# Optimization experiments

Measured on AMD Instinct MI355X. Metric: run time of the kernel, lower is better.

The kernel has to match this reference:

```python
import jax, jax.numpy as jnp
import numpy as np

D_K = 64

def setup_inputs() -> dict:
    key = jax.random.key(0)
    k1, k2, k3 = jax.random.split(key, 3)
    shape = (4, 16, 2048, D_K)  # [batch, heads, seq, d_k]
    return {
        "q": jax.random.normal(k1, shape, dtype=jnp.float32),
        "k": jax.random.normal(k2, shape, dtype=jnp.float32),
        "v": jax.random.normal(k3, shape, dtype=jnp.float32),
    }

def reference(q, k, v):
    # scores: [B, H, S, S] = Q K^T / sqrt(d_k)
    scale = 1.0 / jnp.sqrt(jnp.asarray(D_K, dtype=q.dtype))
    scores = jnp.einsum("bhqd,bhkd->bhqk", q, k) * scale
    attn = jax.nn.softmax(scores, axis=-1)
    out = jnp.einsum("bhqk,bhkd->bhqd", attn, v)
    return out
```

## Files before the change

### kernel.cpp

```cpp
#include <hip/hip_runtime.h>


#define S_LEN 2048
#define D_K 64
#define BQ 128
#define BK 64
#define NT (S_LEN / BK)
#define LST 72

typedef __attribute__((ext_vector_type(8))) _Float16 fragh;
typedef __attribute__((ext_vector_type(4))) _Float16 half4v;
typedef __attribute__((ext_vector_type(2))) _Float16 half2v;
typedef __attribute__((ext_vector_type(4))) float facc;

__device__ __forceinline__ half2v pkrtz(float a, float b) {
  return __builtin_bit_cast(half2v, __builtin_amdgcn_cvt_pkrtz(a, b));
}

__global__ __launch_bounds__(256, 4) void sdpa_kernel(
    const float* __restrict__ q, const float* __restrict__ k,
    const float* __restrict__ v, float* __restrict__ out) {
  __shared__ _Float16 QP[BQ][LST];
  __shared__ _Float16 Ks[BK][LST];
  __shared__ _Float16 Vs[D_K][LST];

  const int t = threadIdx.x;
  const int wave = t >> 6;
  const int lane = t & 63;
  const int ln15 = lane & 15;
  const int quad = lane >> 4;

  const int bh = blockIdx.y;
  const int q0 = blockIdx.x * BQ;

  const float* qp = q + ((size_t)bh * S_LEN + q0) * D_K;
  const float* kp = k + (size_t)bh * S_LEN * D_K;
  const float* vp = v + (size_t)bh * S_LEN * D_K;

  const float qs = 0.125f * 1.44269504088896340736f;

  #pragma unroll
  for (int i = 0; i < 8; ++i) {
    int e = i * 1024 + t * 4;
    float4 f = *(const float4*)(qp + e);
    int r = e >> 6, c = e & 63;
    half2v a = pkrtz(f.x * qs, f.y * qs);
    half2v b = pkrtz(f.z * qs, f.w * qs);
    *(half4v*)&QP[r][c] = __builtin_shufflevector(a, b, 0, 1, 2, 3);
  }
  __syncthreads();

  fragh qf[2][2];
  #pragma unroll
  for (int mi = 0; mi < 2; ++mi) {
    int row = wave * 32 + mi * 16 + ln15;
    qf[mi][0] = *(const fragh*)&QP[row][quad * 8];
    qf[mi][1] = *(const fragh*)&QP[row][32 + quad * 8];
  }

  fragh ones;
  #pragma unroll
  for (int j = 0; j < 8; ++j) ones[j] = (_Float16)1.0f;

  facc O[2][4];
  facc Ol[2];
  #pragma unroll
  for (int mi = 0; mi < 2; ++mi) {
    Ol[mi] = (facc){0.f, 0.f, 0.f, 0.f};
    #pragma unroll
    for (int r = 0; r < 4; ++r) O[mi][r] = (facc){0.f, 0.f, 0.f, 0.f};
  }

  const int vp0 = ln15 + 16 * (wave & 1);
  const int vg0 = quad + 4 * (wave >> 1);

  float4 kpre[4], vpre[4];
  {
    const float* kb = kp;
    const float* vb = vp;
    #pragma unroll
    for (int i = 0; i < 4; ++i) kpre[i] = *(const float4*)(kb + i * 1024 + t * 4);
    #pragma unroll
    for (int i = 0; i < 2; ++i) {
      const float* vsrc = vb + 2 * vp0 * D_K + 4 * (vg0 + 8 * i);
      vpre[2 * i + 0] = *(const float4*)(vsrc);
      vpre[2 * i + 1] = *(const float4*)(vsrc + D_K);
    }
  }

  for (int kt = 0; kt < NT; ++kt) {
    __syncthreads();

    #pragma unroll
    for (int i = 0; i < 4; ++i) {
      int e = i * 1024 + t * 4;
      int r = e >> 6, c = e & 63;
      half2v a = pkrtz(kpre[i].x, kpre[i].y);
      half2v b = pkrtz(kpre[i].z, kpre[i].w);
      *(half4v*)&Ks[r][c] = __builtin_shufflevector(a, b, 0, 1, 2, 3);
    }
    #pragma unroll
    for (int i = 0; i < 2; ++i) {
      int g = vg0 + 8 * i;
      float4 f0 = vpre[2 * i + 0];
      float4 f1 = vpre[2 * i + 1];
      *(half2v*)&Vs[4 * g + 0][2 * vp0] = pkrtz(f0.x, f1.x);
      *(half2v*)&Vs[4 * g + 1][2 * vp0] = pkrtz(f0.y, f1.y);
      *(half2v*)&Vs[4 * g + 2][2 * vp0] = pkrtz(f0.z, f1.z);
      *(half2v*)&Vs[4 * g + 3][2 * vp0] = pkrtz(f0.w, f1.w);
    }
    __syncthreads();

    if (kt + 1 < NT) {
      const float* kb = kp + (kt + 1) * BK * D_K;
      const float* vb = vp + (kt + 1) * BK * D_K;
      #pragma unroll
      for (int i = 0; i < 4; ++i) kpre[i] = *(const float4*)(kb + i * 1024 + t * 4);
      #pragma unroll
      for (int i = 0; i < 2; ++i) {
        const float* vsrc = vb + 2 * vp0 * D_K + 4 * (vg0 + 8 * i);
        vpre[2 * i + 0] = *(const float4*)(vsrc);
        vpre[2 * i + 1] = *(const float4*)(vsrc + D_K);
      }
    }

    #pragma unroll
    for (int kt16 = 0; kt16 < 4; ++kt16) {
      facc s0 = (facc){0.f, 0.f, 0.f, 0.f};
      facc s1 = (facc){0.f, 0.f, 0.f, 0.f};
      #pragma unroll
      for (int ks = 0; ks < 2; ++ks) {
        fragh kf = *(const fragh*)&Ks[kt16 * 16 + ln15][ks * 32 + quad * 8];
        s0 = __builtin_amdgcn_mfma_f32_16x16x32_f16(kf, qf[0][ks], s0, 0, 0, 0);
        s1 = __builtin_amdgcn_mfma_f32_16x16x32_f16(kf, qf[1][ks], s1, 0, 0, 0);
      }
      {
        half2v a = pkrtz(__builtin_amdgcn_exp2f(s0[0]), __builtin_amdgcn_exp2f(s0[1]));
        half2v b = pkrtz(__builtin_amdgcn_exp2f(s0[2]), __builtin_amdgcn_exp2f(s0[3]));
        *(half4v*)&QP[wave * 32 + ln15][kt16 * 16 + quad * 4] =
            __builtin_shufflevector(a, b, 0, 1, 2, 3);
      }
      {
        half2v a = pkrtz(__builtin_amdgcn_exp2f(s1[0]), __builtin_amdgcn_exp2f(s1[1]));
        half2v b = pkrtz(__builtin_amdgcn_exp2f(s1[2]), __builtin_amdgcn_exp2f(s1[3]));
        *(half4v*)&QP[wave * 32 + 16 + ln15][kt16 * 16 + quad * 4] =
            __builtin_shufflevector(a, b, 0, 1, 2, 3);
      }
    }

    fragh pf[2][2];
    #pragma unroll
    for (int mi = 0; mi < 2; ++mi) {
      int row = wave * 32 + mi * 16 + ln15;
      pf[mi][0] = *(const fragh*)&QP[row][quad * 8];
      pf[mi][1] = *(const fragh*)&QP[row][32 + quad * 8];
    }
    #pragma unroll
    for (int ks = 0; ks < 2; ++ks) {
      #pragma unroll
      for (int dt = 0; dt < 4; ++dt) {
        fragh vf = *(const fragh*)&Vs[dt * 16 + ln15][ks * 32 + quad * 8];
        O[0][dt] = __builtin_amdgcn_mfma_f32_16x16x32_f16(vf, pf[0][ks], O[0][dt], 0, 0, 0);
        O[1][dt] = __builtin_amdgcn_mfma_f32_16x16x32_f16(vf, pf[1][ks], O[1][dt], 0, 0, 0);
      }
      Ol[0] = __builtin_amdgcn_mfma_f32_16x16x32_f16(ones, pf[0][ks], Ol[0], 0, 0, 0);
      Ol[1] = __builtin_amdgcn_mfma_f32_16x16x32_f16(ones, pf[1][ks], Ol[1], 0, 0, 0);
    }
  }

  #pragma unroll
  for (int mi = 0; mi < 2; ++mi) {
    float inv = __builtin_amdgcn_rcpf(Ol[mi][0]);
    float* ob = out + ((size_t)bh * S_LEN + q0 + wave * 32 + mi * 16 + ln15) * D_K;
    #pragma unroll
    for (int dt = 0; dt < 4; ++dt) {
      float4 o4;
      o4.x = O[mi][dt][0] * inv;
      o4.y = O[mi][dt][1] * inv;
      o4.z = O[mi][dt][2] * inv;
      o4.w = O[mi][dt][3] * inv;
      *(float4*)&ob[dt * 16 + quad * 4] = o4;
    }
  }
}

extern "C" void kernel_launch(void* const* d_in, const int* in_sizes, int n_in,
                              void* d_out, int out_size, void* d_ws, size_t ws_size,
                              hipStream_t stream) {
  const float* q = (const float*)d_in[0];
  const float* k = (const float*)d_in[1];
  const float* v = (const float*)d_in[2];
  float* out = (float*)d_out;
  dim3 grid(S_LEN / BQ, 64);
  dim3 block(256);
  sdpa_kernel<<<grid, block, 0, stream>>>(q, k, v, out);
}
```

Baseline: 217.4 us.

## Use two waves per block with 64 query rows per wave

```diff
diff --git a/kernel.cpp b/kernel.cpp
--- a/kernel.cpp
+++ b/kernel.cpp
@@ -17,7 +17,7 @@
   return __builtin_bit_cast(half2v, __builtin_amdgcn_cvt_pkrtz(a, b));
 }
 
-__global__ __launch_bounds__(256, 4) void sdpa_kernel(
+__global__ __launch_bounds__(128, 2) void sdpa_kernel(
     const float* __restrict__ q, const float* __restrict__ k,
     const float* __restrict__ v, float* __restrict__ out) {
   __shared__ _Float16 QP[BQ][LST];
@@ -40,8 +40,8 @@
   const float qs = 0.125f * 1.44269504088896340736f;
 
   #pragma unroll
-  for (int i = 0; i < 8; ++i) {
-    int e = i * 1024 + t * 4;
+  for (int i = 0; i < 16; ++i) {
+    int e = i * 512 + t * 4;
     float4 f = *(const float4*)(qp + e);
     int r = e >> 6, c = e & 63;
     half2v a = pkrtz(f.x * qs, f.y * qs);
@@ -50,10 +50,10 @@
   }
   __syncthreads();
 
-  fragh qf[2][2];
+  fragh qf[4][2];
   #pragma unroll
-  for (int mi = 0; mi < 2; ++mi) {
-    int row = wave * 32 + mi * 16 + ln15;
+  for (int mi = 0; mi < 4; ++mi) {
+    int row = wave * 64 + mi * 16 + ln15;
     qf[mi][0] = *(const fragh*)&QP[row][quad * 8];
     qf[mi][1] = *(const fragh*)&QP[row][32 + quad * 8];
   }
@@ -62,27 +62,24 @@
   #pragma unroll
   for (int j = 0; j < 8; ++j) ones[j] = (_Float16)1.0f;
 
-  facc O[2][4];
-  facc Ol[2];
+  facc O[4][4];
+  facc Ol[4];
   #pragma unroll
-  for (int mi = 0; mi < 2; ++mi) {
+  for (int mi = 0; mi < 4; ++mi) {
     Ol[mi] = (facc){0.f, 0.f, 0.f, 0.f};
     #pragma unroll
     for (int r = 0; r < 4; ++r) O[mi][r] = (facc){0.f, 0.f, 0.f, 0.f};
   }
 
   const int vp0 = ln15 + 16 * (wave & 1);
-  const int vg0 = quad + 4 * (wave >> 1);
 
-  float4 kpre[4], vpre[4];
+  float4 kpre[8], vpre[8];
   {
-    const float* kb = kp;
-    const float* vb = vp;
     #pragma unroll
-    for (int i = 0; i < 4; ++i) kpre[i] = *(const float4*)(kb + i * 1024 + t * 4);
+    for (int i = 0; i < 8; ++i) kpre[i] = *(const float4*)(kp + i * 512 + t * 4);
     #pragma unroll
-    for (int i = 0; i < 2; ++i) {
-      const float* vsrc = vb + 2 * vp0 * D_K + 4 * (vg0 + 8 * i);
+    for (int i = 0; i < 4; ++i) {
+      const float* vsrc = vp + 2 * vp0 * D_K + 4 * (quad + 4 * i);
       vpre[2 * i + 0] = *(const float4*)(vsrc);
       vpre[2 * i + 1] = *(const float4*)(vsrc + D_K);
     }
@@ -92,16 +89,16 @@
     __syncthreads();
 
     #pragma unroll
-    for (int i = 0; i < 4; ++i) {
-      int e = i * 1024 + t * 4;
+    for (int i = 0; i < 8; ++i) {
+      int e = i * 512 + t * 4;
       int r = e >> 6, c = e & 63;
       half2v a = pkrtz(kpre[i].x, kpre[i].y);
       half2v b = pkrtz(kpre[i].z, kpre[i].w);
       *(half4v*)&Ks[r][c] = __builtin_shufflevector(a, b, 0, 1, 2, 3);
     }
     #pragma unroll
-    for (int i = 0; i < 2; ++i) {
-      int g = vg0 + 8 * i;
+    for (int i = 0; i < 4; ++i) {
+      int g = quad + 4 * i;
       float4 f0 = vpre[2 * i + 0];
       float4 f1 = vpre[2 * i + 1];
       *(half2v*)&Vs[4 * g + 0][2 * vp0] = pkrtz(f0.x, f1.x);
@@ -115,10 +112,10 @@
       const float* kb = kp + (kt + 1) * BK * D_K;
       const float* vb = vp + (kt + 1) * BK * D_K;
       #pragma unroll
-      for (int i = 0; i < 4; ++i) kpre[i] = *(const float4*)(kb + i * 1024 + t * 4);
+      for (int i = 0; i < 8; ++i) kpre[i] = *(const float4*)(kb + i * 512 + t * 4);
       #pragma unroll
-      for (int i = 0; i < 2; ++i) {
-        const float* vsrc = vb + 2 * vp0 * D_K + 4 * (vg0 + 8 * i);
+      for (int i = 0; i < 4; ++i) {
+        const float* vsrc = vb + 2 * vp0 * D_K + 4 * (quad + 4 * i);
         vpre[2 * i + 0] = *(const float4*)(vsrc);
         vpre[2 * i + 1] = *(const float4*)(vsrc + D_K);
       }
@@ -126,52 +123,48 @@
 
     #pragma unroll
     for (int kt16 = 0; kt16 < 4; ++kt16) {
-      facc s0 = (facc){0.f, 0.f, 0.f, 0.f};
-      facc s1 = (facc){0.f, 0.f, 0.f, 0.f};
+      facc s[4];
+      #pragma unroll
+      for (int mi = 0; mi < 4; ++mi) s[mi] = (facc){0.f, 0.f, 0.f, 0.f};
       #pragma unroll
       for (int ks = 0; ks < 2; ++ks) {
         fragh kf = *(const fragh*)&Ks[kt16 * 16 + ln15][ks * 32 + quad * 8];
-        s0 = __builtin_amdgcn_mfma_f32_16x16x32_f16(kf, qf[0][ks], s0, 0, 0, 0);
-        s1 = __builtin_amdgcn_mfma_f32_16x16x32_f16(kf, qf[1][ks], s1, 0, 0, 0);
+        #pragma unroll
+        for (int mi = 0; mi < 4; ++mi)
+          s[mi] = __builtin_amdgcn_mfma_f32_16x16x32_f16(kf, qf[mi][ks], s[mi], 0, 0, 0);
       }
-      {
-        half2v a = pkrtz(__builtin_amdgcn_exp2f(s0[0]), __builtin_amdgcn_exp2f(s0[1]));
-        half2v b = pkrtz(__builtin_amdgcn_exp2f(s0[2]), __builtin_amdgcn_exp2f(s0[3]));
-        *(half4v*)&QP[wave * 32 + ln15][kt16 * 16 + quad * 4] =
-            __builtin_shufflevector(a, b, 0, 1, 2, 3);
-      }
-      {
-        half2v a = pkrtz(__builtin_amdgcn_exp2f(s1[0]), __builtin_amdgcn_exp2f(s1[1]));
-        half2v b = pkrtz(__builtin_amdgcn_exp2f(s1[2]), __builtin_amdgcn_exp2f(s1[3]));
-        *(half4v*)&QP[wave * 32 + 16 + ln15][kt16 * 16 + quad * 4] =
+      #pragma unroll
+      for (int mi = 0; mi < 4; ++mi) {
+        half2v a = pkrtz(__builtin_amdgcn_exp2f(s[mi][0]), __builtin_amdgcn_exp2f(s[mi][1]));
+        half2v b = pkrtz(__builtin_amdgcn_exp2f(s[mi][2]), __builtin_amdgcn_exp2f(s[mi][3]));
+        *(half4v*)&QP[wave * 64 + mi * 16 + ln15][kt16 * 16 + quad * 4] =
             __builtin_shufflevector(a, b, 0, 1, 2, 3);
       }
     }
 
-    fragh pf[2][2];
-    #pragma unroll
-    for (int mi = 0; mi < 2; ++mi) {
-      int row = wave * 32 + mi * 16 + ln15;
-      pf[mi][0] = *(const fragh*)&QP[row][quad * 8];
-      pf[mi][1] = *(const fragh*)&QP[row][32 + quad * 8];
-    }
     #pragma unroll
     for (int ks = 0; ks < 2; ++ks) {
+      fragh pf[4];
+      #pragma unroll
+      for (int mi = 0; mi < 4; ++mi)
+        pf[mi] = *(const fragh*)&QP[wave * 64 + mi * 16 + ln15][ks * 32 + quad * 8];
       #pragma unroll
       for (int dt = 0; dt < 4; ++dt) {
         fragh vf = *(const fragh*)&Vs[dt * 16 + ln15][ks * 32 + quad * 8];
-        O[0][dt] = __builtin_amdgcn_mfma_f32_16x16x32_f16(vf, pf[0][ks], O[0][dt], 0, 0, 0);
-        O[1][dt] = __builtin_amdgcn_mfma_f32_16x16x32_f16(vf, pf[1][ks], O[1][dt], 0, 0, 0);
+        #pragma unroll
+        for (int mi = 0; mi < 4; ++mi)
+          O[mi][dt] = __builtin_amdgcn_mfma_f32_16x16x32_f16(vf, pf[mi], O[mi][dt], 0, 0, 0);
       }
-      Ol[0] = __builtin_amdgcn_mfma_f32_16x16x32_f16(ones, pf[0][ks], Ol[0], 0, 0, 0);
-      Ol[1] = __builtin_amdgcn_mfma_f32_16x16x32_f16(ones, pf[1][ks], Ol[1], 0, 0, 0);
+      #pragma unroll
+      for (int mi = 0; mi < 4; ++mi)
+        Ol[mi] = __builtin_amdgcn_mfma_f32_16x16x32_f16(ones, pf[mi], Ol[mi], 0, 0, 0);
     }
   }
 
   #pragma unroll
-  for (int mi = 0; mi < 2; ++mi) {
+  for (int mi = 0; mi < 4; ++mi) {
     float inv = __builtin_amdgcn_rcpf(Ol[mi][0]);
-    float* ob = out + ((size_t)bh * S_LEN + q0 + wave * 32 + mi * 16 + ln15) * D_K;
+    float* ob = out + ((size_t)bh * S_LEN + q0 + wave * 64 + mi * 16 + ln15) * D_K;
     #pragma unroll
     for (int dt = 0; dt < 4; ++dt) {
       float4 o4;
@@ -192,6 +185,6 @@
   const float* v = (const float*)d_in[2];
   float* out = (float*)d_out;
   dim3 grid(S_LEN / BQ, 64);
-  dim3 block(256);
+  dim3 block(128);
   sdpa_kernel<<<grid, block, 0, stream>>>(q, k, v, out);
 }
```

After: 204.4 us. -6.0%, faster.
